# Kernel tuning notes

Hardware: AMD Instinct MI355X
Metric: run time of the kernel (lower is better)

The kernel has to match this reference:

```python
import jax, jax.numpy as jnp
import numpy as np

NMOL, BSIZE = 2048, 64
NSP, NCOEF = 500000, 64
L0, NROT, NREP = 100000, 200000, 500000
ROT_LEN = 2 + L0 + NROT * 3  # rot_out = [0,1] ++ direct ++ rotated


def setup_inputs() -> dict:
    key = jax.random.key(0)
    ks = jax.random.split(key, 13)
    A = jax.random.normal(ks[0], (NSP, NCOEF), jnp.float32) * 0.1
    b = jax.random.normal(ks[1], (NSP,), jnp.float32) * 0.1
    coeffs = jax.random.normal(ks[2], (NCOEF,), jnp.float32) * 0.1
    rot_tensor = jax.random.normal(ks[3], (NROT, 3, 3), jnp.float32)
    Sr = jax.random.normal(ks[4], (NMOL, BSIZE, BSIZE), jnp.float32)
    S = jnp.eye(BSIZE, dtype=jnp.float32) + 0.02 * (Sr + Sr.transpose(0, 2, 1))  # SPD overlap
    Gr = jax.random.normal(ks[5], (NMOL, BSIZE, BSIZE), jnp.float32)
    G = 0.5 * (Gr + Gr.transpose(0, 2, 1))  # symmetric Gamma
    rho = jax.random.normal(ks[6], (NMOL, BSIZE, BSIZE), jnp.float32) * 0.1
    qneutral = jax.random.uniform(ks[7], (NMOL, BSIZE, 1), jnp.float32)
    nocc = BSIZE // 2  # occupied orbital columns
    occ_mask = jnp.broadcast_to((jnp.arange(BSIZE) < nocc).astype(jnp.float32)[None, None, :],
                                (NMOL, BSIZE, BSIZE))
    g_rot_direct = jax.random.randint(ks[8], (L0,), 0, NSP)
    g_rot = jax.random.randint(ks[9], (NROT * 3,), 0, NSP)
    g_oper = jax.random.randint(ks[10], (NMOL * BSIZE * BSIZE,), 0, ROT_LEN)
    g_rep = jax.random.randint(ks[11], (NREP,), 0, NSP)
    seg_ids = jnp.sort(jax.random.randint(ks[12], (NREP,), 0, NMOL))
    return dict(A=A, b=b, coeffs=coeffs, rot_tensor=rot_tensor, S=S, G=G, rho=rho,
                qneutral=qneutral, occ_mask=occ_mask, g_rot_direct=g_rot_direct,
                g_rot=g_rot, g_oper=g_oper, g_rep=g_rep, seg_ids=seg_ids)


def reference(A, b, coeffs, rot_tensor, S, G, rho, qneutral, occ_mask,
              g_rot_direct, g_rot, g_oper, g_rep, seg_ids):
    nmol, bsize, _ = S.shape
    # spline evaluation: net_vals = A @ coeffs + b  (form_initial_layer / vals)
    net_vals = A @ coeffs + b  # [NSP]
    # rotation stage: direct gather + batched 3x3 rotation of gathered 3-vectors
    rotated = jnp.einsum('nij,nj->ni', rot_tensor, net_vals[g_rot].reshape(-1, 3)).ravel()
    rot_out = jnp.concatenate([jnp.array([0.0, 1.0], dtype=net_vals.dtype),
                               net_vals[g_rot_direct], rotated])  # [ROT_LEN]
    # operator matrix reconstruction via irregular gather
    H = rot_out[g_oper].reshape(nmol, bsize, bsize)
    # Mulliken charges and Coulomb matrix
    qbasis = rho * S
    GOP = jnp.sum(qbasis, axis=2, keepdims=True)        # [nmol,bsize,1]
    dQ = qneutral - GOP
    ep = G @ dQ                                          # [nmol,bsize,1]
    couMat = -0.5 * S * (ep + ep.transpose(0, 2, 1))
    F = H + couMat
    # repulsive energy: fused segment sum (replaces the python-loop segment sum)
    Erep = jax.ops.segment_sum(net_vals[g_rep], seg_ids, num_segments=nmol)
    # generalized eigenproblem via Loewdin orthogonalization (phiS = S^{-1/2})
    Svals, Svecs = jnp.linalg.eigh(S)
    phiS = Svecs * (Svals ** -0.5)[:, None, :]
    fockp = phiS.transpose(0, 2, 1) @ F @ phiS
    Eorb, C = jnp.linalg.eigh(fockp)                     # [nmol,bsize], [nmol,bsize,bsize]
    orb = phiS @ C
    orb_filled = occ_mask * orb
    rho_out = 2.0 * orb_filled @ orb_filled.transpose(0, 2, 1)
    # electronic energy
    ener1 = jnp.sum(rho_out * H, axis=(1, 2))
    ener2 = 0.5 * jnp.sum(dQ * (G @ dQ), axis=(1, 2))
    Eelec = ener1 + ener2
    Etot = Eelec + Erep
    return jnp.concatenate([Etot[:, None], Eorb], axis=1)  # [nmol, bsize+1]
```

## Files before the change

kernel.cpp:

```cpp
#include <hip/hip_runtime.h>


#define NMOLC 2048
#define NSPC  500000
#define L0C   100000
#define NROTC 200000
#define NREPC 500000
#define MS 68

__global__ __launch_bounds__(256) void k_netvals(const float* __restrict__ A,
                                                 const float* __restrict__ b,
                                                 const float* __restrict__ coeffs,
                                                 float* __restrict__ net){
  int gid = blockIdx.x * 256 + threadIdx.x;
  int row = gid >> 4;
  int l   = gid & 15;
  if (row >= NSPC) return;
  float4 c4 = reinterpret_cast<const float4*>(coeffs)[l];
  float4 a4 = reinterpret_cast<const float4*>(A)[(size_t)row * 16 + l];
  float s = a4.x*c4.x + a4.y*c4.y + a4.z*c4.z + a4.w*c4.w;
  s += __shfl_xor(s, 1, 16);
  s += __shfl_xor(s, 2, 16);
  s += __shfl_xor(s, 4, 16);
  s += __shfl_xor(s, 8, 16);
  if (l == 0) net[row] = s + b[row];
}

__global__ __launch_bounds__(256) void k_rot(const float* __restrict__ net,
                                             const float* __restrict__ rot_tensor,
                                             const int* __restrict__ g_rot_direct,
                                             const int* __restrict__ g_rot,
                                             float* __restrict__ rot_out){
  int gid = blockIdx.x * 256 + threadIdx.x;
  if (gid == 0){ rot_out[0] = 0.f; rot_out[1] = 1.f; }
  if (gid < L0C){
    rot_out[2 + gid] = net[g_rot_direct[gid]];
  }
  int n = gid - L0C;
  if (n >= 0 && n < NROTC){
    float v0 = net[g_rot[3*n    ]];
    float v1 = net[g_rot[3*n + 1]];
    float v2 = net[g_rot[3*n + 2]];
    const float* R = rot_tensor + (size_t)9 * n;
    float* o = rot_out + 2 + L0C + 3*n;
    o[0] = R[0]*v0 + R[1]*v1 + R[2]*v2;
    o[1] = R[3]*v0 + R[4]*v1 + R[5]*v2;
    o[2] = R[6]*v0 + R[7]*v1 + R[8]*v2;
  }
}

__global__ __launch_bounds__(256) void k_coulomb(const float* __restrict__ S,
                                                 const float* __restrict__ G,
                                                 const float* __restrict__ rho,
                                                 const float* __restrict__ qneutral,
                                                 float* __restrict__ ep_all,
                                                 float* __restrict__ ener2_a,
                                                 float* __restrict__ erep_a){
  __shared__ float sRed[256];
  __shared__ float sdQ[64];
  __shared__ float sEp[64];
  const int mol = blockIdx.x;
  const int t = threadIdx.x;
  const int i = t >> 2, q4 = t & 3;
  const float* Sm = S   + (size_t)mol * 4096;
  const float* Gm = G   + (size_t)mol * 4096;
  const float* Rm = rho + (size_t)mol * 4096;

  float acc = 0.f;
  {
    const float4* S4 = reinterpret_cast<const float4*>(Sm + i*64 + q4*16);
    const float4* R4 = reinterpret_cast<const float4*>(Rm + i*64 + q4*16);
    #pragma unroll
    for (int m = 0; m < 4; ++m){
      float4 sv = S4[m], rv = R4[m];
      acc += sv.x*rv.x + sv.y*rv.y + sv.z*rv.z + sv.w*rv.w;
    }
  }
  sRed[t] = acc; __syncthreads();
  if (t < 64) sdQ[t] = qneutral[(size_t)mol*64 + t]
                       - (sRed[4*t] + sRed[4*t+1] + sRed[4*t+2] + sRed[4*t+3]);
  __syncthreads();

  float acc2 = 0.f;
  {
    const float4* G4 = reinterpret_cast<const float4*>(Gm + i*64 + q4*16);
    #pragma unroll
    for (int m = 0; m < 4; ++m){
      float4 gv = G4[m];
      int j0 = q4*16 + m*4;
      acc2 += gv.x*sdQ[j0] + gv.y*sdQ[j0+1] + gv.z*sdQ[j0+2] + gv.w*sdQ[j0+3];
    }
  }
  sRed[t] = acc2; __syncthreads();
  if (t < 64){
    float e = sRed[4*t] + sRed[4*t+1] + sRed[4*t+2] + sRed[4*t+3];
    sEp[t] = e;
    ep_all[(size_t)mol*64 + t] = e;
  }
  __syncthreads();
  if (t == 0){
    float s = 0.f;
    for (int j = 0; j < 64; ++j) s += sdQ[j] * sEp[j];
    ener2_a[mol] = 0.5f * s;
    erep_a[mol]  = 0.f;
  }
}

__global__ __launch_bounds__(256) void k_erep(const float* __restrict__ net,
                                              const int* __restrict__ g_rep,
                                              const int* __restrict__ seg_ids,
                                              float* __restrict__ erep_a){
  const int CH = 64;
  long tid = (long)blockIdx.x * 256 + threadIdx.x;
  long start = tid * CH;
  if (start >= NREPC) return;
  long end = start + CH; if (end > NREPC) end = NREPC;
  int cur = seg_ids[start];
  float acc = 0.f;
  for (long e = start; e < end; ++e){
    int sgid = seg_ids[e];
    if (sgid != cur){ atomicAdd(&erep_a[cur], acc); cur = sgid; acc = 0.f; }
    acc += net[g_rep[e]];
  }
  atomicAdd(&erep_a[cur], acc);
}

__device__ __forceinline__ void mm_symA(float (*__restrict__ D)[MS],
                                        const float (*__restrict__ A)[MS],
                                        const float (*__restrict__ B)[MS],
                                        float alpha, float diag, int t){
  const int r0 = (t & 15) << 2, c0 = (t >> 4) << 2;
  float acc[4][4];
  #pragma unroll
  for (int i = 0; i < 4; ++i)
    #pragma unroll
    for (int j = 0; j < 4; ++j) acc[i][j] = 0.f;
  #pragma unroll 8
  for (int k = 0; k < 64; ++k){
    float4 av = *reinterpret_cast<const float4*>(&A[k][r0]);
    float4 bv = *reinterpret_cast<const float4*>(&B[k][c0]);
    float a_[4] = {av.x, av.y, av.z, av.w};
    float b_[4] = {bv.x, bv.y, bv.z, bv.w};
    #pragma unroll
    for (int i = 0; i < 4; ++i)
      #pragma unroll
      for (int j = 0; j < 4; ++j)
        acc[i][j] += a_[i] * b_[j];
  }
  #pragma unroll
  for (int i = 0; i < 4; ++i)
    #pragma unroll
    for (int j = 0; j < 4; ++j)
      D[r0+i][c0+j] = alpha * acc[i][j] + ((r0+i) == (c0+j) ? diag : 0.f);
}

__global__ __launch_bounds__(256, 2) void k_ns(const float* __restrict__ S,
                                               const int* __restrict__ g_oper,
                                               const float* __restrict__ rot_out,
                                               const float* __restrict__ ep_all,
                                               float* __restrict__ fockp_all,
                                               float* __restrict__ C2_all){
  __shared__ float M[4][64][MS];
  __shared__ float sEp[64];
  const int t   = threadIdx.x;
  const int mol = blockIdx.x;
  const float* Sm = S + (size_t)mol * 4096;
  const int*   gm = g_oper + (size_t)mol * 4096;

  #pragma unroll
  for (int m = 0; m < 16; ++m){
    int e = t + (m << 8);
    int i = e >> 6, j = e & 63;
    float s = Sm[e];
    M[0][i][j] = s;
    M[2][i][j] = ((i == j) ? 3.f : 0.f) - s;
  }
  if (t < 64) sEp[t] = ep_all[(size_t)mol*64 + t];
  __syncthreads();
  mm_symA(M[3], M[0], M[2], 0.5f, 0.f, t);
  #pragma unroll
  for (int m = 0; m < 16; ++m){
    int e = t + (m << 8);
    M[1][e >> 6][e & 63] = 0.5f * M[2][e >> 6][e & 63];
  }
  __syncthreads();
  mm_symA(M[0], M[1], M[3], -1.f, 3.f, t); __syncthreads();
  mm_symA(M[2], M[3], M[0], 0.5f, 0.f, t); __syncthreads();
  mm_symA(M[3], M[0], M[1], 0.5f, 0.f, t); __syncthreads();
  mm_symA(M[1], M[3], M[2], -1.f, 3.f, t); __syncthreads();
  mm_symA(M[0], M[1], M[3], 0.5f, 0.f, t); __syncthreads();

  #pragma unroll
  for (int m = 0; m < 16; ++m){
    int e = t + (m << 8);
    M[1][e >> 6][e & 63] = rot_out[gm[e]];
  }
  __syncthreads();
  #pragma unroll
  for (int m = 0; m < 16; ++m){
    int e = t + (m << 8);
    int i = e >> 6, j = e & 63;
    M[2][i][j] = 0.5f*(M[1][i][j] + M[1][j][i]) - 0.5f*Sm[e]*(sEp[i] + sEp[j]);
  }
  __syncthreads();
  mm_symA(M[3], M[2], M[0], 1.f, 0.f, t); __syncthreads();
  mm_symA(M[1], M[0], M[3], 1.f, 0.f, t); __syncthreads();
  #pragma unroll
  for (int m = 0; m < 16; ++m){
    int e = t + (m << 8);
    fockp_all[(size_t)mol * 4096 + e] = M[1][e >> 6][e & 63];
  }
  #pragma unroll
  for (int m = 0; m < 16; ++m){
    int e = t + (m << 8);
    M[2][e >> 6][e & 63] = Sm[e];
  }
  __syncthreads();
  mm_symA(M[3], M[2], M[0], 1.f, 0.f, t); __syncthreads();
  #pragma unroll
  for (int m = 0; m < 16; ++m){
    int e = t + (m << 8);
    int i = e >> 6, j = e & 63;
    M[3][i][j] *= sEp[i];
  }
  __syncthreads();
  mm_symA(M[1], M[0], M[3], 1.f, 0.f, t); __syncthreads();
  #pragma unroll
  for (int m = 0; m < 16; ++m){
    int e = t + (m << 8);
    C2_all[(size_t)mol * 4096 + e] = M[1][e >> 6][e & 63];
  }
}

__global__ __launch_bounds__(64, 2) void k_jac(const float* __restrict__ fockp_all,
                                               const float* __restrict__ C2_all,
                                               const float* __restrict__ ener2_a,
                                               const float* __restrict__ erep_a,
                                               float* __restrict__ out){
  __shared__ float Bl[64 * 68];
  const int lane = threadIdx.x;
  const int mol  = blockIdx.x;
  const float* Am = fockp_all + (size_t)mol * 4096;
  const float* Cm = C2_all    + (size_t)mol * 4096;
  const int pid  = lane & 31;
  const int half = lane >> 5;

  float Ac[32], Bc[32];
  float csA = 0.f, csB = 0.f;
  #pragma unroll
  for (int i = 0; i < 32; ++i){
    float a = Am[(half*32 + i)*64 + pid];
    float b = Am[(half*32 + i)*64 + 32 + pid];
    Ac[i] = a; Bc[i] = b;
    csA += fabsf(a); csB += fabsf(b);
  }
  #pragma unroll
  for (int i = 0; i < 64; ++i) Bl[i*68 + lane] = Cm[i*64 + lane];

  csA += __shfl_xor(csA, 32);
  csB += __shfl_xor(csB, 32);
  float mu = fmaxf(csA, csB);
  #pragma unroll
  for (int d = 1; d < 32; d <<= 1) mu = fmaxf(mu, __shfl_xor(mu, d));
  mu *= 1.02f;
  #pragma unroll
  for (int i = 0; i < 32; ++i){
    Ac[i] += (half == 0 && i == pid) ? mu : 0.f;
    Bc[i] += (half == 1 && i == pid) ? mu : 0.f;
  }

  for (int sweep = 0; sweep < 4; ++sweep){
    float al = 0.f, bl = 0.f;
    #pragma unroll
    for (int i = 0; i < 32; ++i){
      al = fmaf(Ac[i], Ac[i], al);
      bl = fmaf(Bc[i], Bc[i], bl);
    }
    float alpha = al + __shfl_xor(al, 32);
    float beta  = bl + __shfl_xor(bl, 32);

    unsigned long long any = 0ULL;
    for (int j = 5; j >= 0; --j){
      const int M = 1 << j;
      for (int k = 0; k < M; ++k){
        float gl = 0.f;
        #pragma unroll
        for (int i = 0; i < 32; ++i) gl = fmaf(Ac[i], Bc[i], gl);
        float gamma = gl + __shfl_xor(gl, 32);
        bool rot = (gamma * gamma) > (1e-9f * alpha * beta);
        unsigned long long bal = __ballot(rot);
        any |= bal;
        if (bal != 0ULL){
          float tau = (beta - alpha) / (2.f * gamma);
          float tq  = copysignf(1.f, tau) / (fabsf(tau) + sqrtf(fmaf(tau, tau, 1.f)));
          float c = rsqrtf(fmaf(tq, tq, 1.f));
          float s = tq * c;
          if (!rot){ c = 1.f; s = 0.f; }
          float na = c*c*alpha + s*s*beta - 2.f*c*s*gamma;
          float nb = s*s*alpha + c*c*beta + 2.f*c*s*gamma;
          alpha = na; beta = nb;
          #pragma unroll
          for (int i = 0; i < 32; ++i){
            float ta = Ac[i];
            Ac[i] = fmaf(-s, Bc[i], c * ta);
            Bc[i] = fmaf( c, Bc[i], s * ta);
          }
        }
        if (k < M - 1){
          int e  = k ^ (k >> 1);
          int e2 = (k + 1) ^ ((k + 1) >> 1);
          int mig = e ^ e2;
          #pragma unroll
          for (int i = 0; i < 32; ++i) Bc[i] = __shfl_xor(Bc[i], mig);
          beta = __shfl_xor(beta, mig);
        } else if (j > 0){
          const int Mp = M >> 1;
          const bool hb = (pid & Mp) != 0;
          #pragma unroll
          for (int i = 0; i < 32; ++i){
            float send = hb ? Ac[i] : Bc[i];
            float recv = __shfl_xor(send, Mp);
            Ac[i] = hb ? Bc[i] : Ac[i];
            Bc[i] = recv;
          }
          float sendb = hb ? alpha : beta;
          float recvb = __shfl_xor(sendb, Mp);
          alpha = hb ? beta : alpha;
          beta  = recvb;
        }
      }
    }
    if (any == 0ULL) break;
  }

  float nA = 0.f, nB = 0.f;
  #pragma unroll
  for (int i = 0; i < 32; ++i){
    nA = fmaf(Ac[i], Ac[i], nA);
    nB = fmaf(Bc[i], Bc[i], nB);
  }
  nA += __shfl_xor(nA, 32);
  nB += __shfl_xor(nB, 32);
  float myLamS = half ? sqrtf(nB) : sqrtf(nA);
  float myLam  = myLamS - mu;

  int rank = 0;
  for (int k = 0; k < 64; ++k){
    float lk = __shfl(myLam, k);
    rank += (lk < myLam || (lk == myLam && k < lane)) ? 1 : 0;
  }
  out[(size_t)mol*65 + 1 + rank] = myLam;

  float occf = (rank < 32) ? 1.f : 0.f;
  float slam = occf * myLam;
  #pragma unroll
  for (int d = 1; d < 64; d <<= 1) slam += __shfl_xor(slam, d);

  float myScale = occf / myLamS;
  float sA = __shfl(myScale, pid);
  float sB = __shfl(myScale, 32 + pid);
  #pragma unroll
  for (int i = 0; i < 32; ++i){ Ac[i] *= sA; Bc[i] *= sB; }

  __syncthreads();

  const int myB = half * 32;
  const int otB = 32 - myB;
  float pv[32];
  float term = 0.f;
  #pragma unroll
  for (int i = 0; i < 32; ++i) pv[i] = __shfl_xor(Ac[i], 32);
  #pragma unroll 4
  for (int i = 0; i < 32; ++i){
    const float* row = &Bl[(myB + i) * 68];
    float d = 0.f;
    #pragma unroll
    for (int k = 0; k < 32; k += 4){
      float4 c1 = *reinterpret_cast<const float4*>(&row[myB + k]);
      d = fmaf(c1.x, Ac[k], d);   d = fmaf(c1.y, Ac[k+1], d);
      d = fmaf(c1.z, Ac[k+2], d); d = fmaf(c1.w, Ac[k+3], d);
      float4 c2 = *reinterpret_cast<const float4*>(&row[otB + k]);
      d = fmaf(c2.x, pv[k], d);   d = fmaf(c2.y, pv[k+1], d);
      d = fmaf(c2.z, pv[k+2], d); d = fmaf(c2.w, pv[k+3], d);
    }
    term = fmaf(Ac[i], d, term);
  }
  #pragma unroll
  for (int i = 0; i < 32; ++i) pv[i] = __shfl_xor(Bc[i], 32);
  #pragma unroll 4
  for (int i = 0; i < 32; ++i){
    const float* row = &Bl[(myB + i) * 68];
    float d = 0.f;
    #pragma unroll
    for (int k = 0; k < 32; k += 4){
      float4 c1 = *reinterpret_cast<const float4*>(&row[myB + k]);
      d = fmaf(c1.x, Bc[k], d);   d = fmaf(c1.y, Bc[k+1], d);
      d = fmaf(c1.z, Bc[k+2], d); d = fmaf(c1.w, Bc[k+3], d);
      float4 c2 = *reinterpret_cast<const float4*>(&row[otB + k]);
      d = fmaf(c2.x, pv[k], d);   d = fmaf(c2.y, pv[k+1], d);
      d = fmaf(c2.z, pv[k+2], d); d = fmaf(c2.w, pv[k+3], d);
    }
    term = fmaf(Bc[i], d, term);
  }
  #pragma unroll
  for (int d2 = 1; d2 < 64; d2 <<= 1) term += __shfl_xor(term, d2);

  if (lane == 0){
    out[(size_t)mol*65] = 2.f*slam + 2.f*term + ener2_a[mol] + erep_a[mol];
  }
}

extern "C" void kernel_launch(void* const* d_in, const int* in_sizes, int n_in,
                              void* d_out, int out_size, void* d_ws, size_t ws_size,
                              hipStream_t stream){
  (void)in_sizes; (void)n_in; (void)out_size; (void)ws_size;
  const float* A          = (const float*)d_in[0];
  const float* b          = (const float*)d_in[1];
  const float* coeffs     = (const float*)d_in[2];
  const float* rot_tensor = (const float*)d_in[3];
  const float* S          = (const float*)d_in[4];
  const float* G          = (const float*)d_in[5];
  const float* rho        = (const float*)d_in[6];
  const float* qneutral   = (const float*)d_in[7];
  const int* g_rot_direct = (const int*)d_in[9];
  const int* g_rot        = (const int*)d_in[10];
  const int* g_oper       = (const int*)d_in[11];
  const int* g_rep        = (const int*)d_in[12];
  const int* seg_ids      = (const int*)d_in[13];
  float* out = (float*)d_out;

  float* W         = (float*)d_ws;
  float* net       = W;
  float* rot_out   = W + 500000;
  float* ep_all    = W + 1200004;
  float* ener2_a   = W + 1331076;
  float* erep_a    = W + 1333124;
  float* fockp_all = W + 1335172;
  float* C2_all    = W + 9723780;

  k_netvals<<<(NSPC*16)/256, 256, 0, stream>>>(A, b, coeffs, net);
  k_rot<<<(L0C + NROTC + 255)/256, 256, 0, stream>>>(net, rot_tensor, g_rot_direct, g_rot, rot_out);
  k_coulomb<<<NMOLC, 256, 0, stream>>>(S, G, rho, qneutral, ep_all, ener2_a, erep_a);
  k_erep<<<((NREPC + 63)/64 + 255)/256, 256, 0, stream>>>(net, g_rep, seg_ids, erep_a);
  k_ns<<<NMOLC, 256, 0, stream>>>(S, g_oper, rot_out, ep_all, fockp_all, C2_all);
  k_jac<<<NMOLC, 64, 0, stream>>>(fockp_all, C2_all, ener2_a, erep_a, out);
}
```

Before: 582.6 us.

## Trim Jacobi sweeps, split dot-product accumulators, use fast intrinsics and shear rotations

Drops the one-sided Jacobi eigen solver from 4 to 3 sweeps. Splits the serial dot-product reductions into 4 independent accumulators to shorten the FMA dependency chains. Replaces the IEEE divides and sqrt with AMDGCN rcp/sqrt/rsq intrinsics. Applies each rotation as three shear passes (tangent of the half-angle) instead of the two-multiply form. Cutting a sweep lowers the work per molecule but may leave eigenvalues less converged, and the approximate intrinsics and shear form change rounding.

Measured after the change: 513.9 us, median of 3. 11.8% less time.

```diff
diff --git a/kernel.cpp b/kernel.cpp
--- a/kernel.cpp
+++ b/kernel.cpp
@@ -269,42 +269,55 @@
     Bc[i] += (half == 1 && i == pid) ? mu : 0.f;
   }
 
-  for (int sweep = 0; sweep < 4; ++sweep){
-    float al = 0.f, bl = 0.f;
-    #pragma unroll
-    for (int i = 0; i < 32; ++i){
-      al = fmaf(Ac[i], Ac[i], al);
-      bl = fmaf(Bc[i], Bc[i], bl);
-    }
-    float alpha = al + __shfl_xor(al, 32);
-    float beta  = bl + __shfl_xor(bl, 32);
+  for (int sweep = 0; sweep < 3; ++sweep){
+    float a0 = 0.f, a1 = 0.f, a2 = 0.f, a3 = 0.f;
+    float b0 = 0.f, b1 = 0.f, b2 = 0.f, b3 = 0.f;
+    #pragma unroll
+    for (int i = 0; i < 32; i += 4){
+      a0 = fmaf(Ac[i],   Ac[i],   a0); a1 = fmaf(Ac[i+1], Ac[i+1], a1);
+      a2 = fmaf(Ac[i+2], Ac[i+2], a2); a3 = fmaf(Ac[i+3], Ac[i+3], a3);
+      b0 = fmaf(Bc[i],   Bc[i],   b0); b1 = fmaf(Bc[i+1], Bc[i+1], b1);
+      b2 = fmaf(Bc[i+2], Bc[i+2], b2); b3 = fmaf(Bc[i+3], Bc[i+3], b3);
+    }
+    float alpha = (a0 + a1) + (a2 + a3);
+    float beta  = (b0 + b1) + (b2 + b3);
+    alpha += __shfl_xor(alpha, 32);
+    beta  += __shfl_xor(beta, 32);
 
     unsigned long long any = 0ULL;
     for (int j = 5; j >= 0; --j){
       const int M = 1 << j;
       for (int k = 0; k < M; ++k){
-        float gl = 0.f;
+        float g0 = 0.f, g1 = 0.f, g2 = 0.f, g3 = 0.f;
         #pragma unroll
-        for (int i = 0; i < 32; ++i) gl = fmaf(Ac[i], Bc[i], gl);
-        float gamma = gl + __shfl_xor(gl, 32);
+        for (int i = 0; i < 32; i += 4){
+          g0 = fmaf(Ac[i],   Bc[i],   g0);
+          g1 = fmaf(Ac[i+1], Bc[i+1], g1);
+          g2 = fmaf(Ac[i+2], Bc[i+2], g2);
+          g3 = fmaf(Ac[i+3], Bc[i+3], g3);
+        }
+        float gamma = (g0 + g1) + (g2 + g3);
+        gamma += __shfl_xor(gamma, 32);
         bool rot = (gamma * gamma) > (1e-9f * alpha * beta);
         unsigned long long bal = __ballot(rot);
         any |= bal;
         if (bal != 0ULL){
-          float tau = (beta - alpha) / (2.f * gamma);
-          float tq  = copysignf(1.f, tau) / (fabsf(tau) + sqrtf(fmaf(tau, tau, 1.f)));
-          float c = rsqrtf(fmaf(tq, tq, 1.f));
+          float tau = (beta - alpha) * 0.5f * __builtin_amdgcn_rcpf(gamma);
+          float tq  = copysignf(1.f, tau) *
+                      __builtin_amdgcn_rcpf(fabsf(tau) + __builtin_amdgcn_sqrtf(fmaf(tau, tau, 1.f)));
+          float c = __builtin_amdgcn_rsqf(fmaf(tq, tq, 1.f));
           float s = tq * c;
-          if (!rot){ c = 1.f; s = 0.f; }
+          float th = s * __builtin_amdgcn_rcpf(1.f + c);
+          if (!rot){ c = 1.f; s = 0.f; th = 0.f; }
           float na = c*c*alpha + s*s*beta - 2.f*c*s*gamma;
           float nb = s*s*alpha + c*c*beta + 2.f*c*s*gamma;
           alpha = na; beta = nb;
           #pragma unroll
-          for (int i = 0; i < 32; ++i){
-            float ta = Ac[i];
-            Ac[i] = fmaf(-s, Bc[i], c * ta);
-            Bc[i] = fmaf( c, Bc[i], s * ta);
-          }
+          for (int i = 0; i < 32; ++i) Ac[i] = fmaf(-th, Bc[i], Ac[i]);
+          #pragma unroll
+          for (int i = 0; i < 32; ++i) Bc[i] = fmaf( s,  Ac[i], Bc[i]);
+          #pragma unroll
+          for (int i = 0; i < 32; ++i) Ac[i] = fmaf(-th, Bc[i], Ac[i]);
         }
         if (k < M - 1){
           int e  = k ^ (k >> 1);
@@ -333,12 +346,15 @@
     if (any == 0ULL) break;
   }
 
-  float nA = 0.f, nB = 0.f;
-  #pragma unroll
-  for (int i = 0; i < 32; ++i){
-    nA = fmaf(Ac[i], Ac[i], nA);
-    nB = fmaf(Bc[i], Bc[i], nB);
-  }
+  float nA0 = 0.f, nA1 = 0.f, nB0 = 0.f, nB1 = 0.f;
+  #pragma unroll
+  for (int i = 0; i < 32; i += 2){
+    nA0 = fmaf(Ac[i],   Ac[i],   nA0);
+    nA1 = fmaf(Ac[i+1], Ac[i+1], nA1);
+    nB0 = fmaf(Bc[i],   Bc[i],   nB0);
+    nB1 = fmaf(Bc[i+1], Bc[i+1], nB1);
+  }
+  float nA = nA0 + nA1, nB = nB0 + nB1;
   nA += __shfl_xor(nA, 32);
   nB += __shfl_xor(nB, 32);
   float myLamS = half ? sqrtf(nB) : sqrtf(nA);
```
